# Optimization experiments

Measured on AMD Instinct MI355X. Metric: run time of the kernel, lower is better.

Reference implementation:

```python
import jax, jax.numpy as jnp
import numpy as np

B, N, M, D = 16, 4096, 4096, 3


def setup_inputs() -> dict:
    key = jax.random.key(0)
    k1, k2 = jax.random.split(key)
    xyz1 = jax.random.normal(k1, (B, N, D), dtype=jnp.float32)
    xyz2 = jax.random.normal(k2, (B, M, D), dtype=jnp.float32)
    return {"xyz1": xyz1, "xyz2": xyz2}


def _chamfer(xyz1, xyz2):
    # Squared pairwise distances via ||a||^2 + ||b||^2 - 2 a.b  -> [B, N, M]
    s1 = jnp.sum(xyz1 * xyz1, axis=-1)                     # [B, N]
    s2 = jnp.sum(xyz2 * xyz2, axis=-1)                     # [B, M]
    cross = jnp.einsum("bnd,bmd->bnm", xyz1, xyz2)        # [B, N, M]
    d2 = s1[:, :, None] + s2[:, None, :] - 2.0 * cross
    d2 = jnp.maximum(d2, 0.0)  # guard tiny negatives from cancellation
    dist1 = jnp.min(d2, axis=2)  # nearest point in set2 for each point in set1, [B, N]
    dist2 = jnp.min(d2, axis=1)  # nearest point in set1 for each point in set2, [B, M]
    return dist1, dist2


def reference(xyz1, xyz2):
    return _chamfer(xyz1, xyz2)
```

## Files before the change

kernel.cpp:

```cpp
#include <hip/hip_runtime.h>

typedef _Float16 h8     __attribute__((ext_vector_type(8)));
typedef float    f32x16 __attribute__((ext_vector_type(16)));

#define BB      16
#define NPTS    4096
#define WAVES   4
#define RPW     64
#define RPB     (WAVES * RPW)
#define CSPLIT  2
#define COLS    (NPTS / CSPLIT)
#define CHUNK   512
#define NCHUNK  (COLS / CHUNK)
#define NT      (CHUNK / 32)
#define SEGS    4
#define TPB     (WAVES * 64)

__global__ __launch_bounds__(256) void chamfer_prep(
    const float* __restrict__ xyz1, const float* __restrict__ xyz2,
    _Float16* __restrict__ Aws, _Float16* __restrict__ Bws,
    float* __restrict__ out)
{
    const int idx = blockIdx.x * 256 + threadIdx.x;
    out[idx] = 3.0e38f;
    const int s   = idx >> 16;
    const int rem = idx & 65535;
    const float* p = (s == 0 ? xyz1 : xyz2) + rem * 3;
    float x = p[0], y = p[1], z = p[2];
    float ss = fmaf(x, x, fmaf(y, y, z * z));
    _Float16 xh = (_Float16)x, yh = (_Float16)y, zh = (_Float16)z;
    _Float16 xl = (_Float16)(x - (float)xh);
    _Float16 yl = (_Float16)(y - (float)yh);
    _Float16 zl = (_Float16)(z - (float)zh);
    _Float16 sh = (_Float16)ss;
    _Float16 sl = (_Float16)(ss - (float)sh);
    _Float16 one = (_Float16)1.0f, zero = (_Float16)0.0f;
    _Float16 m2xh = (_Float16)(-2.0f) * xh;
    _Float16 m2yh = (_Float16)(-2.0f) * yh;
    _Float16 m2zh = (_Float16)(-2.0f) * zh;
    _Float16 m2xl = (_Float16)(-2.0f * (x - (float)xh));
    _Float16 m2yl = (_Float16)(-2.0f * (y - (float)yh));
    _Float16 m2zl = (_Float16)(-2.0f * (z - (float)zh));

    _Float16* A = Aws + (size_t)idx * 16;
    *(h8*)(A)     = h8{xh, yh, zh, xh, yh, zh, xl, yl};
    *(h8*)(A + 8) = h8{zl, sh, sl, one, one, zero, zero, zero};

    const int pp = idx & 4095;
    const int slab = idx >> 12;
    _Float16* B = Bws + (size_t)slab * (NPTS * 16) + (pp >> 5) * 512 + (pp & 31) * 8;
    *(h8*)(B)       = h8{m2xh, m2yh, m2zh, m2xl, m2yl, m2zl, m2xh, m2yh};
    *(h8*)(B + 256) = h8{m2zh, one, one, sh, sl, zero, zero, zero};
}

__global__ __launch_bounds__(TPB, 4) void chamfer_mfma(
    const _Float16* __restrict__ Aws,
    const _Float16* __restrict__ Bws,
    float* __restrict__ out)
{
    __shared__ __align__(16) _Float16 sb[2][CHUNK * 16];

    const int tid  = threadIdx.x;
    const int lane = tid & 63;
    const int wv   = tid >> 6;
    const int rb   = blockIdx.x;
    const int b    = blockIdx.y;
    const int z    = blockIdx.z;
    const int dir  = z & 1;
    const int csp  = z >> 1;

    h8 af0, af1;
    {
        const _Float16* Abase = Aws + ((size_t)dir << 20) + (size_t)b * (NPTS * 16);
        const int r0 = rb * RPB + wv * RPW + (lane & 31);
        const int hs = (lane >> 5) * 8;
        af0 = *(const h8*)(Abase + (size_t)r0 * 16 + hs);
        af1 = *(const h8*)(Abase + (size_t)(r0 + 32) * 16 + hs);
    }
    const _Float16* Bbase = Bws + ((size_t)(dir ^ 1) << 20) + (size_t)b * (NPTS * 16)
                          + (size_t)csp * (COLS * 16);

    const f32x16 Z = {};
    float rm0[16], rm1[16];
#pragma unroll
    for (int r = 0; r < 16; ++r) { rm0[r] = 3.0e38f; rm1[r] = 3.0e38f; }

    const int loff = ((lane >> 5) << 8) + (lane & 31) * 8;

    auto stage = [&](int ch, int buf) {
        const char* g = (const char*)(Bbase + (size_t)ch * CHUNK * 16);
        char* l = (char*)&sb[buf][0];
#pragma unroll
        for (int j = 0; j < SEGS; ++j) {
            int seg = wv * SEGS + j;
            __builtin_amdgcn_global_load_lds(
                (const unsigned int*)(g + seg * 1024 + lane * 16),
                (unsigned int*)(l + seg * 1024), 16, 0, 0);
        }
    };

    auto sweep = [&](int buf) {
        const _Float16* base = &sb[buf][0];
#pragma unroll 1
        for (int t = 0; t < NT; t += 2) {
            h8 bx = *(const h8*)(base + t * 512 + loff);
            h8 by = *(const h8*)(base + (t + 1) * 512 + loff);
            f32x16 c0 = __builtin_amdgcn_mfma_f32_32x32x16_f16(af0, bx, Z, 0, 0, 0);
            f32x16 c1 = __builtin_amdgcn_mfma_f32_32x32x16_f16(af0, by, Z, 0, 0, 0);
            f32x16 d0 = __builtin_amdgcn_mfma_f32_32x32x16_f16(af1, bx, Z, 0, 0, 0);
            f32x16 d1 = __builtin_amdgcn_mfma_f32_32x32x16_f16(af1, by, Z, 0, 0, 0);
#pragma unroll
            for (int r = 0; r < 16; ++r)
                rm0[r] = fminf(fminf(c0[r], c1[r]), rm0[r]);
#pragma unroll
            for (int r = 0; r < 16; ++r)
                rm1[r] = fminf(fminf(d0[r], d1[r]), rm1[r]);
        }
    };

    stage(0, 0);
    __syncthreads();
#pragma unroll 1
    for (int ch = 0; ch < NCHUNK; ++ch) {
        int buf = ch & 1;
        if (ch + 1 < NCHUNK) stage(ch + 1, buf ^ 1);
        sweep(buf);
        __syncthreads();
    }

#pragma unroll
    for (int r = 0; r < 16; ++r) {
        float m = rm0[r];
        m = fminf(m, __shfl_xor(m, 1));
        m = fminf(m, __shfl_xor(m, 2));
        m = fminf(m, __shfl_xor(m, 4));
        m = fminf(m, __shfl_xor(m, 8));
        m = fminf(m, __shfl_xor(m, 16));
        rm0[r] = m;
        float n = rm1[r];
        n = fminf(n, __shfl_xor(n, 1));
        n = fminf(n, __shfl_xor(n, 2));
        n = fminf(n, __shfl_xor(n, 4));
        n = fminf(n, __shfl_xor(n, 8));
        n = fminf(n, __shfl_xor(n, 16));
        rm1[r] = n;
    }
    if ((lane & 31) == 0) {
        const int half = lane >> 5;
        int* o = (int*)out + dir * (BB * NPTS) + b * NPTS + rb * RPB + wv * RPW;
#pragma unroll
        for (int r = 0; r < 16; ++r) {
            int rr = (r & 3) + 8 * (r >> 2) + 4 * half;
            atomicMin(o + rr,      __float_as_int(fmaxf(rm0[r], 0.0f)));
            atomicMin(o + 32 + rr, __float_as_int(fmaxf(rm1[r], 0.0f)));
        }
    }
}

extern "C" void kernel_launch(void* const* d_in, const int* in_sizes, int n_in,
                              void* d_out, int out_size, void* d_ws, size_t ws_size,
                              hipStream_t stream) {
    const float* xyz1 = (const float*)d_in[0];
    const float* xyz2 = (const float*)d_in[1];
    float* out = (float*)d_out;
    _Float16* Aws = (_Float16*)d_ws;
    _Float16* Bws = Aws + (size_t)2 * BB * NPTS * 16;

    hipLaunchKernelGGL(chamfer_prep, dim3(2 * BB * NPTS / 256), dim3(256), 0, stream,
                       xyz1, xyz2, Aws, Bws, out);

    dim3 grid(NPTS / RPB, BB, 2 * CSPLIT);
    hipLaunchKernelGGL(chamfer_mfma, grid, dim3(TPB), 0, stream, Aws, Bws, out);
}
```

Measured before the change: 36.85 us.

## Halve rows per wave, shrink chunks, and remap blocks onto XCDs by slab

Each wave now handles 32 rows with a single A fragment instead of 64, the LDS chunk drops to 256 columns, and launch bounds allow 8 blocks per CU. The 3D grid becomes a 1D grid whose block index is decoded so that all row blocks of one (batch, direction, column-split) slab land on the same XCD, aiming for better L2 locality of the B tiles. This doubles the block count and lowers register pressure to raise occupancy. In exchange each loaded B fragment now feeds one MFMA instead of two, and the number of LDS staging rounds and atomics per output row rises.

```diff
diff --git a/kernel.cpp b/kernel.cpp
--- a/kernel.cpp
+++ b/kernel.cpp
@@ -6,15 +6,17 @@
 #define BB      16
 #define NPTS    4096
 #define WAVES   4
-#define RPW     64
+#define RPW     32
 #define RPB     (WAVES * RPW)
 #define CSPLIT  2
 #define COLS    (NPTS / CSPLIT)
-#define CHUNK   512
+#define CHUNK   256
 #define NCHUNK  (COLS / CHUNK)
 #define NT      (CHUNK / 32)
-#define SEGS    4
+#define SEGS    2
 #define TPB     (WAVES * 64)
+#define NSLAB   (2 * BB * CSPLIT)
+#define RBLK    (NPTS / RPB)
 
 __global__ __launch_bounds__(256) void chamfer_prep(
     const float* __restrict__ xyz1, const float* __restrict__ xyz2,
@@ -53,7 +55,7 @@
     *(h8*)(B + 256) = h8{m2zh, one, one, sh, sl, zero, zero, zero};
 }
 
-__global__ __launch_bounds__(TPB, 4) void chamfer_mfma(
+__global__ __launch_bounds__(TPB, 8) void chamfer_mfma(
     const _Float16* __restrict__ Aws,
     const _Float16* __restrict__ Bws,
     float* __restrict__ out)
@@ -63,27 +65,29 @@
     const int tid  = threadIdx.x;
     const int lane = tid & 63;
     const int wv   = tid >> 6;
-    const int rb   = blockIdx.x;
-    const int b    = blockIdx.y;
-    const int z    = blockIdx.z;
-    const int dir  = z & 1;
-    const int csp  = z >> 1;
 
-    h8 af0, af1;
+    const int wgid   = blockIdx.x;
+    const int xcd    = wgid & 7;
+    const int within = wgid >> 3;
+    const int rb     = within & (RBLK - 1);
+    const int slab   = (within >> 5) * 8 + xcd;
+    const int dir    = slab & 1;
+    const int b      = (slab >> 1) & (BB - 1);
+    const int csp    = slab >> 5;
+
+    h8 af;
     {
         const _Float16* Abase = Aws + ((size_t)dir << 20) + (size_t)b * (NPTS * 16);
-        const int r0 = rb * RPB + wv * RPW + (lane & 31);
-        const int hs = (lane >> 5) * 8;
-        af0 = *(const h8*)(Abase + (size_t)r0 * 16 + hs);
-        af1 = *(const h8*)(Abase + (size_t)(r0 + 32) * 16 + hs);
+        const int row = rb * RPB + wv * RPW + (lane & 31);
+        af = *(const h8*)(Abase + (size_t)row * 16 + (lane >> 5) * 8);
     }
     const _Float16* Bbase = Bws + ((size_t)(dir ^ 1) << 20) + (size_t)b * (NPTS * 16)
                           + (size_t)csp * (COLS * 16);
 
     const f32x16 Z = {};
-    float rm0[16], rm1[16];
+    float rm[16];
 #pragma unroll
-    for (int r = 0; r < 16; ++r) { rm0[r] = 3.0e38f; rm1[r] = 3.0e38f; }
+    for (int r = 0; r < 16; ++r) rm[r] = 3.0e38f;
 
     const int loff = ((lane >> 5) << 8) + (lane & 31) * 8;
 
@@ -102,19 +106,12 @@
     auto sweep = [&](int buf) {
         const _Float16* base = &sb[buf][0];
 #pragma unroll 1
-        for (int t = 0; t < NT; t += 2) {
-            h8 bx = *(const h8*)(base + t * 512 + loff);
-            h8 by = *(const h8*)(base + (t + 1) * 512 + loff);
-            f32x16 c0 = __builtin_amdgcn_mfma_f32_32x32x16_f16(af0, bx, Z, 0, 0, 0);
-            f32x16 c1 = __builtin_amdgcn_mfma_f32_32x32x16_f16(af0, by, Z, 0, 0, 0);
-            f32x16 d0 = __builtin_amdgcn_mfma_f32_32x32x16_f16(af1, bx, Z, 0, 0, 0);
-            f32x16 d1 = __builtin_amdgcn_mfma_f32_32x32x16_f16(af1, by, Z, 0, 0, 0);
+        for (int t = 0; t < NT; ++t) {
+            h8 bt = *(const h8*)(base + t * 512 + loff);
+            f32x16 c = __builtin_amdgcn_mfma_f32_32x32x16_f16(af, bt, Z, 0, 0, 0);
 #pragma unroll
             for (int r = 0; r < 16; ++r)
-                rm0[r] = fminf(fminf(c0[r], c1[r]), rm0[r]);
-#pragma unroll
-            for (int r = 0; r < 16; ++r)
-                rm1[r] = fminf(fminf(d0[r], d1[r]), rm1[r]);
+                rm[r] = fminf(c[r], rm[r]);
         }
     };
 
@@ -130,20 +127,13 @@
 
 #pragma unroll
     for (int r = 0; r < 16; ++r) {
-        float m = rm0[r];
+        float m = rm[r];
         m = fminf(m, __shfl_xor(m, 1));
         m = fminf(m, __shfl_xor(m, 2));
         m = fminf(m, __shfl_xor(m, 4));
         m = fminf(m, __shfl_xor(m, 8));
         m = fminf(m, __shfl_xor(m, 16));
-        rm0[r] = m;
-        float n = rm1[r];
-        n = fminf(n, __shfl_xor(n, 1));
-        n = fminf(n, __shfl_xor(n, 2));
-        n = fminf(n, __shfl_xor(n, 4));
-        n = fminf(n, __shfl_xor(n, 8));
-        n = fminf(n, __shfl_xor(n, 16));
-        rm1[r] = n;
+        rm[r] = m;
     }
     if ((lane & 31) == 0) {
         const int half = lane >> 5;
@@ -151,8 +141,7 @@
 #pragma unroll
         for (int r = 0; r < 16; ++r) {
             int rr = (r & 3) + 8 * (r >> 2) + 4 * half;
-            atomicMin(o + rr,      __float_as_int(fmaxf(rm0[r], 0.0f)));
-            atomicMin(o + 32 + rr, __float_as_int(fmaxf(rm1[r], 0.0f)));
+            atomicMin(o + rr, __float_as_int(fmaxf(rm[r], 0.0f)));
         }
     }
 }
@@ -169,6 +158,6 @@
     hipLaunchKernelGGL(chamfer_prep, dim3(2 * BB * NPTS / 256), dim3(256), 0, stream,
                        xyz1, xyz2, Aws, Bws, out);
 
-    dim3 grid(NPTS / RPB, BB, 2 * CSPLIT);
-    hipLaunchKernelGGL(chamfer_mfma, grid, dim3(TPB), 0, stream, Aws, Bws, out);
+    hipLaunchKernelGGL(chamfer_mfma, dim3(RBLK * NSLAB), dim3(TPB), 0, stream,
+                       Aws, Bws, out);
 }
```

Result: slower. 64.55 us (+75.2%).
